# Optimization experiments

Measured on AMD Instinct MI355X. Metric: run time of the kernel, lower is better.

The kernel has to match this reference:

```python
import jax, jax.numpy as jnp
import numpy as np


def setup_inputs() -> dict:
    key = jax.random.key(0)
    k1, k2 = jax.random.split(key)
    xyz1 = jax.random.normal(k1, (4, 8192, 3), dtype=jnp.float32)
    xyz2 = jax.random.normal(k2, (4, 8192, 3), dtype=jnp.float32)
    return {"xyz1": xyz1, "xyz2": xyz2}


def reference(xyz1, xyz2):
    # Pairwise squared distances ||p - q||^2 = |p|^2 + |q|^2 - 2 p.q
    # Avoids materializing the (B, N, M, 3) difference tensor the torch code builds.
    sq1 = jnp.sum(xyz1 * xyz1, axis=-1)                      # (B, N)
    sq2 = jnp.sum(xyz2 * xyz2, axis=-1)                      # (B, M)
    cross = jnp.einsum('bnc,bmc->bnm', xyz1, xyz2)           # (B, N, M)
    dist = sq1[:, :, None] + sq2[:, None, :] - 2.0 * cross   # (B, N, M)
    dist1 = jnp.min(dist, axis=2)                            # (B, N)
    dist2 = jnp.min(dist, axis=1)                            # (B, M)
    return (dist1, dist2)
```

## Files before the change

kernel.cpp:

```cpp
#include <hip/hip_runtime.h>
#include <float.h>

#define BATCH 4

typedef _Float16 half8 __attribute__((ext_vector_type(8)));
typedef float f32x16 __attribute__((ext_vector_type(16)));
typedef float f32x2 __attribute__((ext_vector_type(2)));


__global__ void prep_fp16(const float* __restrict__ x1, const float* __restrict__ x2,
                          _Float16* __restrict__ pa1, _Float16* __restrict__ pb1,
                          _Float16* __restrict__ pa2, _Float16* __restrict__ pb2,
                          float* __restrict__ out, int n1, int n2, int outn) {
    const int i = blockIdx.x * blockDim.x + threadIdx.x;
    const _Float16 one = (_Float16)1.0f, zro = (_Float16)0.0f;

    #pragma unroll
    for (int which = 0; which < 2; ++which) {
        const int n = which ? n2 : n1;
        if (i >= n) continue;
        const float* xp = (which ? x2 : x1) + 3 * (size_t)i;
        _Float16* pa = (which ? pa2 : pa1) + 16 * (size_t)i;
        _Float16* pb = (which ? pb2 : pb1) + 16 * (size_t)i;

        const float x = xp[0], y = xp[1], z = xp[2];
        const _Float16 hx = (_Float16)x, hy = (_Float16)y, hz = (_Float16)z;
        const _Float16 ex = (_Float16)(x - (float)hx);
        const _Float16 ey = (_Float16)(y - (float)hy);
        const _Float16 ez = (_Float16)(z - (float)hz);
        const float ps = fmaf(x, x, fmaf(y, y, z * z));
        const _Float16 ph = (_Float16)ps;
        const _Float16 pe = (_Float16)(ps - (float)ph);
        const _Float16 tx = (_Float16)(-2.0f * (float)hx);
        const _Float16 ty = (_Float16)(-2.0f * (float)hy);
        const _Float16 tz = (_Float16)(-2.0f * (float)hz);
        const _Float16 ux = (_Float16)(-2.0f * (float)ex);
        const _Float16 uy = (_Float16)(-2.0f * (float)ey);
        const _Float16 uz = (_Float16)(-2.0f * (float)ez);

        const half8 a0 = (half8){hx, hy, hz, hx, hy, hz, ex, ey};
        const half8 a1 = (half8){ez, ph, pe, one, one, zro, zro, zro};
        const half8 b0 = (half8){tx, ty, tz, ux, uy, uz, tx, ty};
        const half8 b1 = (half8){tz, one, one, ph, pe, zro, zro, zro};

        *(half8*)(pa)     = a0;
        *(half8*)(pa + 8) = a1;
        *(half8*)(pb)     = b0;
        *(half8*)(pb + 8) = b1;
    }
    if (i < outn) out[i] = FLT_MAX;
}

__device__ inline float min16(const f32x16 d) {
    const float t0 = fminf(fminf(d[0],  d[1]),  d[2]);
    const float t1 = fminf(fminf(d[3],  d[4]),  d[5]);
    const float t2 = fminf(fminf(d[6],  d[7]),  d[8]);
    const float t3 = fminf(fminf(d[9],  d[10]), d[11]);
    const float t4 = fminf(fminf(d[12], d[13]), d[14]);
    const float u0 = fminf(fminf(t0, t1), t2);
    const float u1 = fminf(fminf(t3, t4), d[15]);
    return fminf(u0, u1);
}

template<int NJ>
__global__ __launch_bounds__(256) void chamfer_mfma32(
        const _Float16* __restrict__ pa1, const _Float16* __restrict__ pb1,
        const _Float16* __restrict__ pa2, const _Float16* __restrict__ pb2,
        float* __restrict__ out, int N) {
    constexpr int IT = 2;
    __shared__ uint4 sA[512];

    const int tid  = threadIdx.x;
    const int lane = tid & 63;
    const int w    = tid >> 6;

    int bid = blockIdx.x;
    const int RB      = N / 256;
    const int per_dir = BATCH * RB * NJ;
    const int dir = bid / per_dir;   bid %= per_dir;
    const int b   = bid / (RB * NJ); bid %= (RB * NJ);
    const int cb  = bid / NJ;
    const int js  = bid % NJ;

    const _Float16* pstage = dir ? pa1 : pa2;
    const _Float16* pheld  = dir ? pb2 : pb1;
    float* outd = out + (size_t)dir * BATCH * N + (size_t)b * N;

    const int colbase = cb * 256 + w * 64;
    const uint4* gh = (const uint4*)pheld;
    half8 bf[IT];
    #pragma unroll
    for (int it = 0; it < IT; ++it) {
        const int c = colbase + it * 32 + (lane & 31);
        bf[it] = __builtin_bit_cast(half8, gh[(size_t)(b * N + c) * 2 + (lane >> 5)]);
    }

    float rmin[IT];
    #pragma unroll
    for (int it = 0; it < IT; ++it) rmin[it] = FLT_MAX;

    f32x16 cz;
    #pragma unroll
    for (int e = 0; e < 16; ++e) cz[e] = 0.0f;

    const int jseg   = N / NJ;
    const int stages = jseg / 256;
    const uint4* gs  = (const uint4*)pstage;
    const int t = tid >> 5, col = tid & 31;

    for (int s = 0; s < stages; ++s) {
        const size_t q = (size_t)(b * N + js * jseg + s * 256 + tid) * 2;
        const uint4 v0 = gs[q];
        const uint4 v1 = gs[q + 1];
        __syncthreads();
        sA[t * 64 + col]      = v0;
        sA[t * 64 + 32 + col] = v1;
        __syncthreads();

        #pragma unroll
        for (int p = 0; p < 8; ++p) {
            const half8 a = __builtin_bit_cast(half8, sA[p * 64 + lane]);
            #pragma unroll
            for (int it = 0; it < IT; ++it) {
                const f32x16 d = __builtin_amdgcn_mfma_f32_32x32x16_f16(a, bf[it], cz, 0, 0, 0);
                rmin[it] = fminf(rmin[it], min16(d));
            }
        }
    }

    #pragma unroll
    for (int it = 0; it < IT; ++it) {
        float v = fminf(rmin[it], __shfl_xor(rmin[it], 32, 64));
        v = fmaxf(v, 0.0f);
        if (lane < 32)
            atomicMin((int*)&outd[colbase + it * 32 + lane], __float_as_int(v));
    }
}

__global__ void chamfer_prep(const float* __restrict__ xyz1,
                             const float* __restrict__ xyz2,
                             float4* __restrict__ pk1,
                             float4* __restrict__ pk2,
                             float* __restrict__ out,
                             int n1, int n2, int out_n) {
    int i = blockIdx.x * blockDim.x + threadIdx.x;
    if (i < n1) {
        float x = xyz1[3 * (size_t)i], y = xyz1[3 * (size_t)i + 1], z = xyz1[3 * (size_t)i + 2];
        pk1[i] = make_float4(-2.f * x, -2.f * y, -2.f * z, fmaf(x, x, fmaf(y, y, z * z)));
    }
    if (i < n2) {
        float x = xyz2[3 * (size_t)i], y = xyz2[3 * (size_t)i + 1], z = xyz2[3 * (size_t)i + 2];
        pk2[i] = make_float4(-2.f * x, -2.f * y, -2.f * z, fmaf(x, x, fmaf(y, y, z * z)));
    }
    if (i < out_n) out[i] = FLT_MAX;
}

template<int TPB, int CHUNK, int P>
__global__ __launch_bounds__(TPB) void chamfer_fused(
        const float* __restrict__ xyz1, const float* __restrict__ xyz2,
        const float4* __restrict__ pk1, const float4* __restrict__ pk2,
        float* __restrict__ out, int N, int M, int blocks_dir0) {
    __shared__ float4 s[CHUNK];
    int bid = blockIdx.x;
    const int dir = (bid >= blocks_dir0) ? 1 : 0;
    if (dir) bid -= blocks_dir0;
    const int Nsrc = dir ? M : N;
    const int Mdst = dir ? N : M;
    const float* src   = dir ? xyz2 : xyz1;
    const float4* dstp = dir ? pk1  : pk2;
    float* outd        = dir ? (out + (size_t)BATCH * N) : out;
    const int YT = Nsrc / (TPB * P);
    const int Z  = Mdst / CHUNK;
    const int b  = bid / (YT * Z);
    const int r  = bid % (YT * Z);
    const int yt = r / Z;
    const int z  = r % Z;
    const float4* dchunk = dstp + (size_t)b * Mdst + (size_t)z * CHUNK;
    for (int t = threadIdx.x; t < CHUNK / 2; t += TPB) {
        const float4 q0 = dchunk[2 * t];
        const float4 q1 = dchunk[2 * t + 1];
        s[2 * t]     = make_float4(q0.x, q1.x, q0.y, q1.y);
        s[2 * t + 1] = make_float4(q0.z, q1.z, q0.w, q1.w);
    }
    const int i0 = yt * (TPB * P) + threadIdx.x;
    f32x2 px[P], py[P], pz[P];
    float psq[P], m[P];
    #pragma unroll
    for (int k = 0; k < P; ++k) {
        const int i = i0 + k * TPB;
        const float* p = src + ((size_t)b * Nsrc + i) * 3;
        const float x = p[0], y = p[1], zc = p[2];
        px[k] = (f32x2){x, x}; py[k] = (f32x2){y, y}; pz[k] = (f32x2){zc, zc};
        psq[k] = fmaf(x, x, fmaf(y, y, zc * zc));
        m[k] = FLT_MAX;
    }
    __syncthreads();
    #pragma unroll 8
    for (int jj = 0; jj < CHUNK / 2; ++jj) {
        const float4 A = s[2 * jj];
        const float4 B = s[2 * jj + 1];
        const f32x2 xq = (f32x2){A.x, A.y};
        const f32x2 yq = (f32x2){A.z, A.w};
        const f32x2 zq = (f32x2){B.x, B.y};
        const f32x2 wq = (f32x2){B.z, B.w};
        #pragma unroll
        for (int k = 0; k < P; ++k) {
            const f32x2 e = __builtin_elementwise_fma(xq, px[k],
                             __builtin_elementwise_fma(yq, py[k],
                              __builtin_elementwise_fma(zq, pz[k], wq)));
            m[k] = fminf(fminf(m[k], e.x), e.y);
        }
    }
    #pragma unroll
    for (int k = 0; k < P; ++k) {
        const int i = i0 + k * TPB;
        const float d = fmaxf(psq[k] + m[k], 0.0f);
        atomicMin((int*)&outd[(size_t)b * Nsrc + i], __float_as_int(d));
    }
}

extern "C" void kernel_launch(void* const* d_in, const int* in_sizes, int n_in,
                              void* d_out, int out_size, void* d_ws, size_t ws_size,
                              hipStream_t stream) {
    const float* xyz1 = (const float*)d_in[0];
    const float* xyz2 = (const float*)d_in[1];
    float* out = (float*)d_out;

    const int N = in_sizes[0] / (BATCH * 3);
    const int M = in_sizes[1] / (BATCH * 3);
    const int n1 = BATCH * N, n2 = BATCH * M;

    constexpr int TPB = 256;
    constexpr int NJ = 8;

    const size_t need16 = ((size_t)n1 + (size_t)n2) * 64;
    const bool mfma_ok = (N == M) && (N % (NJ * 256) == 0) && (ws_size >= need16);

    if (mfma_ok) {
        _Float16* pa1 = (_Float16*)d_ws;
        _Float16* pb1 = pa1 + (size_t)n1 * 16;
        _Float16* pa2 = pb1 + (size_t)n1 * 16;
        _Float16* pb2 = pa2 + (size_t)n2 * 16;
        int prep_n = out_size > n1 ? out_size : n1;
        if (n2 > prep_n) prep_n = n2;
        prep_fp16<<<(prep_n + TPB - 1) / TPB, TPB, 0, stream>>>(
            xyz1, xyz2, pa1, pb1, pa2, pb2, out, n1, n2, out_size);

        const int grid = 2 * BATCH * (N / 256) * NJ;
        chamfer_mfma32<NJ><<<grid, TPB, 0, stream>>>(pa1, pb1, pa2, pb2, out, N);
        return;
    }

    constexpr int CHUNK = 128;
    constexpr int P = 8;
    const size_t need = ((size_t)n1 + (size_t)n2) * sizeof(float4);
    if (ws_size >= need && (N % (TPB * P) == 0) && (M % (TPB * P) == 0) &&
        (N % CHUNK == 0) && (M % CHUNK == 0)) {
        float4* pk1 = (float4*)d_ws;
        float4* pk2 = pk1 + n1;
        int prep_n = out_size > n1 ? out_size : n1;
        if (n2 > prep_n) prep_n = n2;
        chamfer_prep<<<(prep_n + TPB - 1) / TPB, TPB, 0, stream>>>(
            xyz1, xyz2, pk1, pk2, out, n1, n2, out_size);
        const int blocks_dir0 = BATCH * (N / (TPB * P)) * (M / CHUNK);
        const int blocks_dir1 = BATCH * (M / (TPB * P)) * (N / CHUNK);
        chamfer_fused<TPB, CHUNK, P><<<blocks_dir0 + blocks_dir1, TPB, 0, stream>>>(
            xyz1, xyz2, pk1, pk2, out, N, M, blocks_dir0);
    }
}
```

Measured before the change: 36.50 us.

## Stream A fragments directly from global memory instead of staging through LDS

Removes the shared-memory staging buffer and both block-wide barriers per stage. Each wave now loads its own 32-point A fragment straight from global memory (L2/L1-cached) every tile. The loop is unrolled by 2 to hide load latency. The running min is also folded into the reduction tree. This removes sync and LDS traffic, but every wave in the block now issues redundant global loads and latency is less hidden.

Result: slower. 38.35 us (+5.1%).

```diff
diff --git a/kernel.cpp b/kernel.cpp
--- a/kernel.cpp
+++ b/kernel.cpp
@@ -51,7 +51,7 @@
     if (i < outn) out[i] = FLT_MAX;
 }
 
-__device__ inline float min16(const f32x16 d) {
+__device__ inline float min16_into(float r, const f32x16 d) {
     const float t0 = fminf(fminf(d[0],  d[1]),  d[2]);
     const float t1 = fminf(fminf(d[3],  d[4]),  d[5]);
     const float t2 = fminf(fminf(d[6],  d[7]),  d[8]);
@@ -59,7 +59,7 @@
     const float t4 = fminf(fminf(d[12], d[13]), d[14]);
     const float u0 = fminf(fminf(t0, t1), t2);
     const float u1 = fminf(fminf(t3, t4), d[15]);
-    return fminf(u0, u1);
+    return fminf(fminf(r, u0), u1);
 }
 
 template<int NJ>
@@ -68,7 +68,6 @@
         const _Float16* __restrict__ pa2, const _Float16* __restrict__ pb2,
         float* __restrict__ out, int N) {
     constexpr int IT = 2;
-    __shared__ uint4 sA[512];
 
     const int tid  = threadIdx.x;
     const int lane = tid & 63;
@@ -82,8 +81,8 @@
     const int cb  = bid / NJ;
     const int js  = bid % NJ;
 
-    const _Float16* pstage = dir ? pa1 : pa2;
-    const _Float16* pheld  = dir ? pb2 : pb1;
+    const _Float16* pstream = dir ? pa1 : pa2;
+    const _Float16* pheld   = dir ? pb2 : pb1;
     float* outd = out + (size_t)dir * BATCH * N + (size_t)b * N;
 
     const int colbase = cb * 256 + w * 64;
@@ -104,27 +103,18 @@
     for (int e = 0; e < 16; ++e) cz[e] = 0.0f;
 
     const int jseg   = N / NJ;
-    const int stages = jseg / 256;
-    const uint4* gs  = (const uint4*)pstage;
-    const int t = tid >> 5, col = tid & 31;
-
-    for (int s = 0; s < stages; ++s) {
-        const size_t q = (size_t)(b * N + js * jseg + s * 256 + tid) * 2;
-        const uint4 v0 = gs[q];
-        const uint4 v1 = gs[q + 1];
-        __syncthreads();
-        sA[t * 64 + col]      = v0;
-        sA[t * 64 + 32 + col] = v1;
-        __syncthreads();
-
+    const int ntiles = jseg / 32;
+    const uint4* gs  = (const uint4*)pstream;
+    const size_t abase = (size_t)(b * N + js * jseg) * 2
+                       + (size_t)(lane & 31) * 2 + (lane >> 5);
+
+    #pragma unroll 2
+    for (int tt = 0; tt < ntiles; ++tt) {
+        const half8 a = __builtin_bit_cast(half8, gs[abase + (size_t)tt * 64]);
         #pragma unroll
-        for (int p = 0; p < 8; ++p) {
-            const half8 a = __builtin_bit_cast(half8, sA[p * 64 + lane]);
-            #pragma unroll
-            for (int it = 0; it < IT; ++it) {
-                const f32x16 d = __builtin_amdgcn_mfma_f32_32x32x16_f16(a, bf[it], cz, 0, 0, 0);
-                rmin[it] = fminf(rmin[it], min16(d));
-            }
+        for (int it = 0; it < IT; ++it) {
+            const f32x16 d = __builtin_amdgcn_mfma_f32_32x32x16_f16(a, bf[it], cz, 0, 0, 0);
+            rmin[it] = min16_into(rmin[it], d);
         }
     }
 
```
